# Optimization experiments

Hardware: AMD Instinct MI355X
Metric: run time of the kernel (lower is better)

## Reference

```python
import jax, jax.numpy as jnp
import numpy as np
from jax import lax

R = 4                 # radius (init kwarg)
EPS = 2.0             # eps (init kwarg)
K = 2 * R + 1         # stencil size


def _dir_kernels():
    """8 directional box kernels [8,1,K,K]: L,R,U,D,NW,NE,SW,SE (matches torch construction)."""
    base = np.ones((K, K), np.float32)
    L = base.copy(); L[:, R + 1:] = 0
    Rk = base.copy(); Rk[:, :R] = 0
    U = base.copy(); U[R + 1:, :] = 0
    D = base.copy(); D[:R, :] = 0
    NW = U.copy(); NE = U.copy(); SW = D.copy(); SE = D.copy()
    half = float((R + 1) * (2 * R + 1))
    L, Rk, U, D = L / half, Rk / half, U / half, D / half
    NW[:, R + 1:] = 0; NE[:, :R] = 0; SW[:, R + 1:] = 0; SE[:, :R] = 0
    quad = float((R + 1) ** 2)
    NW, NE, SW, SE = NW / quad, NE / quad, SW / quad, SE / quad
    return jnp.asarray(np.stack([L, Rk, U, D, NW, NE, SW, SE])[:, None])


def _pad(x):
    # ReplicationPad2d(R)
    return jnp.pad(x, ((0, 0), (0, 0), (R, R), (R, R)), mode='edge')


def _conv(x, w, groups=1):
    return lax.conv_general_dilated(
        x, w, window_strides=(1, 1), padding='VALID',
        dimension_numbers=('NCHW', 'OIHW', 'NCHW'), feature_group_count=groups)


def _resize_bilinear_ac(x, H, W):
    """Bilinear resize with align_corners=True, separable gather. x: [N,C,h,w]."""
    n, c, h, w = x.shape
    dt = x.dtype

    def coords(out, src):
        t = jnp.arange(out, dtype=dt) * (jnp.asarray(src - 1, dt) / jnp.asarray(out - 1, dt))
        i0 = jnp.clip(jnp.floor(t).astype(jnp.int32), 0, src - 2)
        f = t - i0.astype(dt)
        return i0, f

    y0, fy = coords(H, h)
    x0, fx = coords(W, w)
    rows = x[:, :, y0, :] * (1 - fy)[None, None, :, None] + x[:, :, y0 + 1, :] * fy[None, None, :, None]
    return rows[:, :, :, x0] * (1 - fx) + rows[:, :, :, x0 + 1] * fx


def setup_inputs() -> dict:
    key = jax.random.key(0)
    k1, k2, k3 = jax.random.split(key, 3)
    lr_x = jax.random.uniform(k1, (1, 3, 256, 256), jnp.float32) * 255.0
    lr_y = jax.random.uniform(k2, (1, 3, 256, 256), jnp.float32) * 255.0
    hr_x = jax.random.uniform(k3, (1, 3, 1024, 1024), jnp.float32) * 255.0
    box_w = jnp.full((3, 1, K, K), 1.0 / (K * K), jnp.float32)  # depthwise box filter weights
    return {"lr_x": lr_x, "lr_y": lr_y, "hr_x": hr_x, "box_w": box_w}


def reference(lr_x, lr_y, hr_x, box_w):
    H, W = hr_x.shape[2], hr_x.shape[3]
    box = lambda t: _conv(_pad(t), box_w, groups=3)

    # --- guided filter coefficients at low res ---
    mean_x = box(lr_x)
    mean_y = box(lr_y)
    cov_xy = box(lr_x * lr_y) - mean_x * mean_y
    var_x = box(lr_x * lr_x) - mean_x * mean_x
    A = cov_xy / (var_x + EPS)
    b = mean_y - A * mean_x

    # --- upsample A, b to hr (bilinear, align_corners=True) ---
    A = _resize_bilinear_ac(A, H, W)
    b = _resize_bilinear_ac(b, H, W)

    # --- 8-direction side-window stencil; channels treated as batch ---
    dirw = _dir_kernels()                      # [8,1,K,K]
    A3 = _pad(A.reshape(3, 1, H, W))
    b3 = _pad(b.reshape(3, 1, H, W))
    im3 = hr_x.reshape(3, 1, H, W)
    cA = _conv(A3, dirw)                       # [3,8,H,W]
    cB = _conv(b3, dirw)                       # [3,8,H,W]
    d = cA * im3 + cB - im3                    # [3,8,H,W]

    idx = jnp.argmin(jnp.abs(d), axis=1, keepdims=True)
    dm = jnp.take_along_axis(d, idx, axis=1)   # min-|delta| direction
    res = (dm + im3).reshape(1, 3, H, W)

    # res.int() truncates toward zero, then clamp(0,255), then float
    return jnp.clip(jnp.trunc(res), 0.0, 255.0)
```

## Files before the change

### kernel.cpp

```cpp
#include <hip/hip_runtime.h>

#define RR 4
#define LRH 256
#define LRW 256
#define HRH 1024
#define HRW 1024

#define LTW 32
#define LTH 8
#define LGW (LTW + 2*RR)
#define LGH (LTH + 2*RR)

#define STW 32
#define STH 32
#define RPT 4
#define SGW (STW + 2*RR)
#define SGH (STH + 2*RR)

__global__ __launch_bounds__(256) void lowres_coeffs(
    const float* __restrict__ lrx, const float* __restrict__ lry,
    float2* __restrict__ AB)
{
    __shared__ float4 sV[LGH][LGW];
    __shared__ float4 sH[LGH][LTW];

    const int c  = blockIdx.z;
    const int X0 = blockIdx.x * LTW, Y0 = blockIdx.y * LTH;
    const int tid = threadIdx.y * LTW + threadIdx.x;
    const float* px = lrx + c * LRH * LRW;
    const float* py = lry + c * LRH * LRW;

    for (int i = tid; i < LGH * LGW; i += 256) {
        int r = i / LGW, col = i - r * LGW;
        int gy = min(max(Y0 - RR + r, 0), LRH - 1);
        int gx = min(max(X0 - RR + col, 0), LRW - 1);
        float xv = px[gy * LRW + gx];
        float yv = py[gy * LRW + gx];
        sV[r][col] = make_float4(xv, yv, xv * yv, xv * xv);
    }
    __syncthreads();

    for (int i = tid; i < LGH * LTW; i += 256) {
        int r = i / LTW, col = i - r * LTW;
        float4 s = sV[r][col];
        #pragma unroll
        for (int k = 1; k < 9; ++k) {
            float4 v = sV[r][col + k];
            s.x += v.x; s.y += v.y; s.z += v.z; s.w += v.w;
        }
        sH[r][col] = s;
    }
    __syncthreads();

    const int tx = threadIdx.x, ty = threadIdx.y;
    float4 s = sH[ty][tx];
    #pragma unroll
    for (int k = 1; k < 9; ++k) {
        float4 v = sH[ty + k][tx];
        s.x += v.x; s.y += v.y; s.z += v.z; s.w += v.w;
    }
    const float inv81 = 1.0f / 81.0f;
    float mx = s.x * inv81, my = s.y * inv81;
    float cov = s.z * inv81 - mx * my;
    float var = s.w * inv81 - mx * mx;
    float A = cov / (var + 2.0f);
    float B = my - A * mx;
    AB[(c * LRH + Y0 + ty) * LRW + X0 + tx] = make_float2(A, B);
}

__global__ __launch_bounds__(256, 4) void stencil_kernel(
    const float2* __restrict__ AB,
    const float* __restrict__ hrx, float* __restrict__ out)
{
    __shared__ float2 sAB[SGH][SGW];
    __shared__ float4 sH[SGH][STW];
    __shared__ int    iLx[SGW];
    __shared__ float2 wLx[SGW];
    __shared__ int    iLyo[SGH];
    __shared__ float2 wLy[SGH];

    const int c  = blockIdx.z;
    const int X0 = blockIdx.x * STW, Y0 = blockIdx.y * STH;
    const int tid = threadIdx.y * STW + threadIdx.x;
    const float2* ABc = AB + c * LRH * LRW;
    const float scale = 255.0f / 1023.0f;

    if (tid < SGW) {
        int gx = min(max(X0 - RR + tid, 0), HRW - 1);
        float t = (float)gx * scale;
        int ix = (int)t; if (ix > LRW - 2) ix = LRW - 2;
        float f = t - (float)ix;
        iLx[tid] = ix;
        wLx[tid] = make_float2(1.0f - f, f);
    } else if (tid >= 64 && tid < 64 + SGH) {
        int r = tid - 64;
        int gy = min(max(Y0 - RR + r, 0), HRH - 1);
        float t = (float)gy * scale;
        int iy = (int)t; if (iy > LRH - 2) iy = LRH - 2;
        float f = t - (float)iy;
        iLyo[r] = iy * LRW;
        wLy[r] = make_float2(1.0f - f, f);
    }
    __syncthreads();

    for (int i = tid; i < SGH * SGW; i += 256) {
        int r = i / SGW, col = i - r * SGW;
        const float2* p = ABc + iLyo[r] + iLx[col];
        float2 wy = wLy[r], wx = wLx[col];
        float2 v00 = p[0], v01 = p[1], v10 = p[LRW], v11 = p[LRW + 1];
        float a0 = v00.x * wy.x + v10.x * wy.y;
        float a1 = v01.x * wy.x + v11.x * wy.y;
        float b0 = v00.y * wy.x + v10.y * wy.y;
        float b1 = v01.y * wy.x + v11.y * wy.y;
        sAB[r][col] = make_float2(a0 * wx.x + a1 * wx.y,
                                  b0 * wx.x + b1 * wx.y);
    }
    __syncthreads();

    for (int i = tid; i < SGH * STW; i += 256) {
        int r = i >> 5, col = i & 31;
        float2 v[9];
        #pragma unroll
        for (int k = 0; k < 9; ++k) v[k] = sAB[r][col + k];
        float hLa = v[0].x + v[1].x + v[2].x + v[3].x + v[4].x;
        float hLb = v[0].y + v[1].y + v[2].y + v[3].y + v[4].y;
        float hRa = v[4].x + v[5].x + v[6].x + v[7].x + v[8].x;
        float hRb = v[4].y + v[5].y + v[6].y + v[7].y + v[8].y;
        sH[r][col] = make_float4(hLa, hLb, hRa, hRb);
    }
    __syncthreads();

    const int tx = threadIdx.x;
    const int base = threadIdx.y * RPT;

    float4 h[RPT + 8];
    float2 cv[RPT + 8];
    #pragma unroll
    for (int k = 0; k < RPT + 8; ++k) {
        h[k]  = sH[base + k][tx];
        cv[k] = sAB[base + k][tx + RR];
    }

    float4 T = h[0], B = h[4];
    float2 Tc = cv[0], Bc = cv[4];
    #pragma unroll
    for (int k = 1; k <= 4; ++k) {
        T.x += h[k].x; T.y += h[k].y; T.z += h[k].z; T.w += h[k].w;
        B.x += h[k+4].x; B.y += h[k+4].y; B.z += h[k+4].z; B.w += h[k+4].w;
        Tc.x += cv[k].x; Tc.y += cv[k].y;
        Bc.x += cv[k+4].x; Bc.y += cv[k+4].y;
    }

    const float i45 = 1.0f / 45.0f, i25 = 1.0f / 25.0f;
    const float* hp = hrx + (c * HRH + Y0 + base) * HRW + X0 + tx;
    float* op = out + (c * HRH + Y0 + base) * HRW + X0 + tx;

    #pragma unroll
    for (int j = 0; j < RPT; ++j) {
        float4 C  = h[j + 4];
        float2 Cc = cv[j + 4];
        float xv = hp[j * HRW];

        float d0 = fmaf(i45, fmaf(T.x + B.x - C.x,  xv, T.y + B.y - C.y),  -xv);
        float d1 = fmaf(i45, fmaf(T.z + B.z - C.z,  xv, T.w + B.w - C.w),  -xv);
        float d2 = fmaf(i45, fmaf(T.x + T.z - Tc.x, xv, T.y + T.w - Tc.y), -xv);
        float d3 = fmaf(i45, fmaf(B.x + B.z - Bc.x, xv, B.y + B.w - Bc.y), -xv);
        float d4 = fmaf(i25, fmaf(T.x, xv, T.y), -xv);
        float d5 = fmaf(i25, fmaf(T.z, xv, T.w), -xv);
        float d6 = fmaf(i25, fmaf(B.x, xv, B.y), -xv);
        float d7 = fmaf(i25, fmaf(B.z, xv, B.w), -xv);

        float a0 = fabsf(d0), a1 = fabsf(d1), a2 = fabsf(d2), a3 = fabsf(d3);
        float a4 = fabsf(d4), a5 = fabsf(d5), a6 = fabsf(d6), a7 = fabsf(d7);
        bool c01 = a0 <= a1; float w01 = c01 ? d0 : d1; float m01 = c01 ? a0 : a1;
        bool c23 = a2 <= a3; float w23 = c23 ? d2 : d3; float m23 = c23 ? a2 : a3;
        bool c45 = a4 <= a5; float w45 = c45 ? d4 : d5; float m45 = c45 ? a4 : a5;
        bool c67 = a6 <= a7; float w67 = c67 ? d6 : d7; float m67 = c67 ? a6 : a7;
        bool cA_ = m01 <= m23; float wA = cA_ ? w01 : w23; float mA = cA_ ? m01 : m23;
        bool cB_ = m45 <= m67; float wB = cB_ ? w45 : w67; float mB = cB_ ? m45 : m67;
        float bd = (mA <= mB) ? wA : wB;

        float res = __builtin_amdgcn_fmed3f(truncf(bd + xv), 0.0f, 255.0f);
        op[j * HRW] = res;

        if (j < RPT - 1) {
            T.x += h[j+5].x - h[j].x;   T.y += h[j+5].y - h[j].y;
            T.z += h[j+5].z - h[j].z;   T.w += h[j+5].w - h[j].w;
            B.x += h[j+9].x - h[j+4].x; B.y += h[j+9].y - h[j+4].y;
            B.z += h[j+9].z - h[j+4].z; B.w += h[j+9].w - h[j+4].w;
            Tc.x += cv[j+5].x - cv[j].x;   Tc.y += cv[j+5].y - cv[j].y;
            Bc.x += cv[j+9].x - cv[j+4].x; Bc.y += cv[j+9].y - cv[j+4].y;
        }
    }
}

extern "C" void kernel_launch(void* const* d_in, const int* in_sizes, int n_in,
                              void* d_out, int out_size, void* d_ws, size_t ws_size,
                              hipStream_t stream) {
    const float* lrx = (const float*)d_in[0];
    const float* lry = (const float*)d_in[1];
    const float* hrx = (const float*)d_in[2];
    (void)d_in[3]; (void)in_sizes; (void)n_in; (void)out_size; (void)ws_size;

    float2* AB = (float2*)d_ws;
    float* outp = (float*)d_out;

    dim3 lblock(LTW, LTH);
    dim3 lgrid(LRW / LTW, LRH / LTH, 3);
    lowres_coeffs<<<lgrid, lblock, 0, stream>>>(lrx, lry, AB);

    dim3 sblock(STW, STH / RPT);
    dim3 sgrid(HRW / STW, HRH / STH, 3);
    stencil_kernel<<<sgrid, sblock, 0, stream>>>(AB, hrx, outp);
}
```

Baseline: 93.54 us.

## Fold bilinear upsampling into directional box sums via precomputed low-res weights

Instead of upsampling A,b to a full high-res halo tile and then box-filtering, the stencil kernel now computes, per output row and column, 4-tap weights that combine the upsample with the half-window box sums. It applies separable vertical weights at low resolution into shared memory (top, bottom and full sums), then horizontal weights per pixel. Tiles grow to 32x64 and occupancy hints rise. This removes the per-tile high-res interpolation and the halo work, but it adds weight-setup loops and different floating-point summation order.

```diff
diff --git a/kernel.cpp b/kernel.cpp
--- a/kernel.cpp
+++ b/kernel.cpp
@@ -1,21 +1,21 @@
 #include <hip/hip_runtime.h>
 
 #define RR 4
-#define LRH 256
-#define LRW 256
-#define HRH 1024
-#define HRW 1024
+#define LRN 256
+#define HRN 1024
+#define SCALE (255.0f/1023.0f)
 
 #define LTW 32
 #define LTH 8
 #define LGW (LTW + 2*RR)
 #define LGH (LTH + 2*RR)
 
-#define STW 32
-#define STH 32
-#define RPT 4
-#define SGW (STW + 2*RR)
-#define SGH (STH + 2*RR)
+#define TX 32
+#define TYR 64
+#define BTH 8
+#define NROW (TYR / BTH)
+#define LRC 12
+#define LRR 20
 
 __global__ __launch_bounds__(256) void lowres_coeffs(
     const float* __restrict__ lrx, const float* __restrict__ lry,
@@ -27,15 +27,15 @@
     const int c  = blockIdx.z;
     const int X0 = blockIdx.x * LTW, Y0 = blockIdx.y * LTH;
     const int tid = threadIdx.y * LTW + threadIdx.x;
-    const float* px = lrx + c * LRH * LRW;
-    const float* py = lry + c * LRH * LRW;
+    const float* px = lrx + c * LRN * LRN;
+    const float* py = lry + c * LRN * LRN;
 
     for (int i = tid; i < LGH * LGW; i += 256) {
         int r = i / LGW, col = i - r * LGW;
-        int gy = min(max(Y0 - RR + r, 0), LRH - 1);
-        int gx = min(max(X0 - RR + col, 0), LRW - 1);
-        float xv = px[gy * LRW + gx];
-        float yv = py[gy * LRW + gx];
+        int gy = min(max(Y0 - RR + r, 0), LRN - 1);
+        int gx = min(max(X0 - RR + col, 0), LRN - 1);
+        float xv = px[gy * LRN + gx];
+        float yv = py[gy * LRN + gx];
         sV[r][col] = make_float4(xv, yv, xv * yv, xv * xv);
     }
     __syncthreads();
@@ -65,110 +65,132 @@
     float var = s.w * inv81 - mx * mx;
     float A = cov / (var + 2.0f);
     float B = my - A * mx;
-    AB[(c * LRH + Y0 + ty) * LRW + X0 + tx] = make_float2(A, B);
-}
-
-__global__ __launch_bounds__(256, 4) void stencil_kernel(
+    AB[(c * LRN + Y0 + ty) * LRN + X0 + tx] = make_float2(A, B);
+}
+
+__device__ inline int anchor_of(int u) {
+    int k = min(max(u - 4, 0), HRN - 1);
+    float t = (float)k * SCALE;
+    int i = (int)t; if (i > LRN - 2) i = LRN - 2;
+    return i;
+}
+
+__device__ inline float4 mkw(int k0, int k1, int a) {
+    float4 w = make_float4(0.f, 0.f, 0.f, 0.f);
+    for (int k = k0; k <= k1; ++k) {
+        int kc = min(max(k, 0), HRN - 1);
+        float t = (float)kc * SCALE;
+        int i = (int)t; if (i > LRN - 2) i = LRN - 2;
+        float f = t - (float)i;
+        int off = i - a;
+        float wa = 1.0f - f, wb = f;
+        w.x += (off == 0) ? wa : 0.0f;
+        w.y += (off == 1) ? wa : ((off == 0) ? wb : 0.0f);
+        w.z += (off == 2) ? wa : ((off == 1) ? wb : 0.0f);
+        w.w += (off == 2) ? wb : 0.0f;
+    }
+    return w;
+}
+
+__global__ __launch_bounds__(256, 6) void stencil_kernel(
     const float2* __restrict__ AB,
     const float* __restrict__ hrx, float* __restrict__ out)
 {
-    __shared__ float2 sAB[SGH][SGW];
-    __shared__ float4 sH[SGH][STW];
-    __shared__ int    iLx[SGW];
-    __shared__ float2 wLx[SGW];
-    __shared__ int    iLyo[SGH];
-    __shared__ float2 wLy[SGH];
+    __shared__ float2 sAB[LRR][LRC];
+    __shared__ float2 sT[TYR][LRC];
+    __shared__ float2 sB[TYR][LRC];
+    __shared__ float2 sF[TYR][LRC];
+    __shared__ float4 sYW[TYR][3];
+    __shared__ int    sYA[TYR];
+    __shared__ float4 sXW[TX][3];
+    __shared__ int    sXA[TX];
 
     const int c  = blockIdx.z;
-    const int X0 = blockIdx.x * STW, Y0 = blockIdx.y * STH;
-    const int tid = threadIdx.y * STW + threadIdx.x;
-    const float2* ABc = AB + c * LRH * LRW;
-    const float scale = 255.0f / 1023.0f;
-
-    if (tid < SGW) {
-        int gx = min(max(X0 - RR + tid, 0), HRW - 1);
-        float t = (float)gx * scale;
-        int ix = (int)t; if (ix > LRW - 2) ix = LRW - 2;
-        float f = t - (float)ix;
-        iLx[tid] = ix;
-        wLx[tid] = make_float2(1.0f - f, f);
-    } else if (tid >= 64 && tid < 64 + SGH) {
+    const int X0 = blockIdx.x * TX, Y0 = blockIdx.y * TYR;
+    const int tid = threadIdx.y * TX + threadIdx.x;
+    const float2* ABc = AB + c * LRN * LRN;
+
+    const int rowbase = anchor_of(Y0);
+    const int colbase = anchor_of(X0);
+
+    if (tid < TX) {
+        int x = X0 + tid;
+        int a = anchor_of(x);
+        sXA[tid] = a - colbase;
+        sXW[tid][0] = mkw(x - 4, x,     a);
+        sXW[tid][1] = mkw(x,     x + 4, a);
+        sXW[tid][2] = mkw(x - 4, x + 4, a);
+    } else if (tid >= 64 && tid < 64 + TYR) {
         int r = tid - 64;
-        int gy = min(max(Y0 - RR + r, 0), HRH - 1);
-        float t = (float)gy * scale;
-        int iy = (int)t; if (iy > LRH - 2) iy = LRH - 2;
-        float f = t - (float)iy;
-        iLyo[r] = iy * LRW;
-        wLy[r] = make_float2(1.0f - f, f);
-    }
-    __syncthreads();
-
-    for (int i = tid; i < SGH * SGW; i += 256) {
-        int r = i / SGW, col = i - r * SGW;
-        const float2* p = ABc + iLyo[r] + iLx[col];
-        float2 wy = wLy[r], wx = wLx[col];
-        float2 v00 = p[0], v01 = p[1], v10 = p[LRW], v11 = p[LRW + 1];
-        float a0 = v00.x * wy.x + v10.x * wy.y;
-        float a1 = v01.x * wy.x + v11.x * wy.y;
-        float b0 = v00.y * wy.x + v10.y * wy.y;
-        float b1 = v01.y * wy.x + v11.y * wy.y;
-        sAB[r][col] = make_float2(a0 * wx.x + a1 * wx.y,
-                                  b0 * wx.x + b1 * wx.y);
-    }
-    __syncthreads();
-
-    for (int i = tid; i < SGH * STW; i += 256) {
-        int r = i >> 5, col = i & 31;
-        float2 v[9];
+        int y = Y0 + r;
+        int a = anchor_of(y);
+        sYA[r] = a - rowbase;
+        sYW[r][0] = mkw(y - 4, y,     a);
+        sYW[r][1] = mkw(y,     y + 4, a);
+        sYW[r][2] = mkw(y - 4, y + 4, a);
+    }
+    for (int i = tid; i < LRR * LRC; i += 256) {
+        int r = i / LRC, cc = i - r * LRC;
+        int gr = min(rowbase + r, LRN - 1);
+        int gc = min(colbase + cc, LRN - 1);
+        sAB[r][cc] = ABc[gr * LRN + gc];
+    }
+    __syncthreads();
+
+    for (int i = tid; i < TYR * LRC; i += 256) {
+        int r = i / LRC, cc = i - r * LRC;
+        int ra = sYA[r];
+        float4 wT = sYW[r][0], wB = sYW[r][1], wF = sYW[r][2];
+        float2 v0 = sAB[ra][cc],     v1 = sAB[ra + 1][cc];
+        float2 v2 = sAB[ra + 2][cc], v3 = sAB[ra + 3][cc];
+        sT[r][cc] = make_float2(wT.x*v0.x + wT.y*v1.x + wT.z*v2.x + wT.w*v3.x,
+                                wT.x*v0.y + wT.y*v1.y + wT.z*v2.y + wT.w*v3.y);
+        sB[r][cc] = make_float2(wB.x*v0.x + wB.y*v1.x + wB.z*v2.x + wB.w*v3.x,
+                                wB.x*v0.y + wB.y*v1.y + wB.z*v2.y + wB.w*v3.y);
+        sF[r][cc] = make_float2(wF.x*v0.x + wF.y*v1.x + wF.z*v2.x + wF.w*v3.x,
+                                wF.x*v0.y + wF.y*v1.y + wF.z*v2.y + wF.w*v3.y);
+    }
+    __syncthreads();
+
+    const int tx = threadIdx.x, tyw = threadIdx.y;
+    const int c0 = sXA[tx];
+    const float4 wL = sXW[tx][0], wR = sXW[tx][1], wFh = sXW[tx][2];
+    const float i45 = 1.0f / 45.0f, i25 = 1.0f / 25.0f;
+    const float* hp = hrx + (c * HRN + Y0 + tyw) * HRN + X0 + tx;
+    float*       op = out + (c * HRN + Y0 + tyw) * HRN + X0 + tx;
+
+    #pragma unroll
+    for (int j = 0; j < NROW; ++j) {
+        const int r = tyw + j * BTH;
+        float LA=0,Lb=0, RA=0,Rb=0, UA=0,Ub=0, DA=0,Db=0;
+        float NWA=0,NWb=0, NEA=0,NEb=0, SWA=0,SWb=0, SEA=0,SEb=0;
         #pragma unroll
-        for (int k = 0; k < 9; ++k) v[k] = sAB[r][col + k];
-        float hLa = v[0].x + v[1].x + v[2].x + v[3].x + v[4].x;
-        float hLb = v[0].y + v[1].y + v[2].y + v[3].y + v[4].y;
-        float hRa = v[4].x + v[5].x + v[6].x + v[7].x + v[8].x;
-        float hRb = v[4].y + v[5].y + v[6].y + v[7].y + v[8].y;
-        sH[r][col] = make_float4(hLa, hLb, hRa, hRb);
-    }
-    __syncthreads();
-
-    const int tx = threadIdx.x;
-    const int base = threadIdx.y * RPT;
-
-    float4 h[RPT + 8];
-    float2 cv[RPT + 8];
-    #pragma unroll
-    for (int k = 0; k < RPT + 8; ++k) {
-        h[k]  = sH[base + k][tx];
-        cv[k] = sAB[base + k][tx + RR];
-    }
-
-    float4 T = h[0], B = h[4];
-    float2 Tc = cv[0], Bc = cv[4];
-    #pragma unroll
-    for (int k = 1; k <= 4; ++k) {
-        T.x += h[k].x; T.y += h[k].y; T.z += h[k].z; T.w += h[k].w;
-        B.x += h[k+4].x; B.y += h[k+4].y; B.z += h[k+4].z; B.w += h[k+4].w;
-        Tc.x += cv[k].x; Tc.y += cv[k].y;
-        Bc.x += cv[k+4].x; Bc.y += cv[k+4].y;
-    }
-
-    const float i45 = 1.0f / 45.0f, i25 = 1.0f / 25.0f;
-    const float* hp = hrx + (c * HRH + Y0 + base) * HRW + X0 + tx;
-    float* op = out + (c * HRH + Y0 + base) * HRW + X0 + tx;
-
-    #pragma unroll
-    for (int j = 0; j < RPT; ++j) {
-        float4 C  = h[j + 4];
-        float2 Cc = cv[j + 4];
-        float xv = hp[j * HRW];
-
-        float d0 = fmaf(i45, fmaf(T.x + B.x - C.x,  xv, T.y + B.y - C.y),  -xv);
-        float d1 = fmaf(i45, fmaf(T.z + B.z - C.z,  xv, T.w + B.w - C.w),  -xv);
-        float d2 = fmaf(i45, fmaf(T.x + T.z - Tc.x, xv, T.y + T.w - Tc.y), -xv);
-        float d3 = fmaf(i45, fmaf(B.x + B.z - Bc.x, xv, B.y + B.w - Bc.y), -xv);
-        float d4 = fmaf(i25, fmaf(T.x, xv, T.y), -xv);
-        float d5 = fmaf(i25, fmaf(T.z, xv, T.w), -xv);
-        float d6 = fmaf(i25, fmaf(B.x, xv, B.y), -xv);
-        float d7 = fmaf(i25, fmaf(B.z, xv, B.w), -xv);
+        for (int k = 0; k < 4; ++k) {
+            float wl = (k==0)?wL.x:(k==1)?wL.y:(k==2)?wL.z:wL.w;
+            float wr = (k==0)?wR.x:(k==1)?wR.y:(k==2)?wR.z:wR.w;
+            float wf = (k==0)?wFh.x:(k==1)?wFh.y:(k==2)?wFh.z:wFh.w;
+            float2 tv = sT[r][c0 + k];
+            float2 bv = sB[r][c0 + k];
+            float2 fv = sF[r][c0 + k];
+            LA = fmaf(wl, fv.x, LA);   Lb = fmaf(wl, fv.y, Lb);
+            RA = fmaf(wr, fv.x, RA);   Rb = fmaf(wr, fv.y, Rb);
+            UA = fmaf(wf, tv.x, UA);   Ub = fmaf(wf, tv.y, Ub);
+            DA = fmaf(wf, bv.x, DA);   Db = fmaf(wf, bv.y, Db);
+            NWA = fmaf(wl, tv.x, NWA); NWb = fmaf(wl, tv.y, NWb);
+            NEA = fmaf(wr, tv.x, NEA); NEb = fmaf(wr, tv.y, NEb);
+            SWA = fmaf(wl, bv.x, SWA); SWb = fmaf(wl, bv.y, SWb);
+            SEA = fmaf(wr, bv.x, SEA); SEb = fmaf(wr, bv.y, SEb);
+        }
+        float xv = hp[j * BTH * HRN];
+
+        float d0 = fmaf(i45, fmaf(LA,  xv, Lb),  -xv);
+        float d1 = fmaf(i45, fmaf(RA,  xv, Rb),  -xv);
+        float d2 = fmaf(i45, fmaf(UA,  xv, Ub),  -xv);
+        float d3 = fmaf(i45, fmaf(DA,  xv, Db),  -xv);
+        float d4 = fmaf(i25, fmaf(NWA, xv, NWb), -xv);
+        float d5 = fmaf(i25, fmaf(NEA, xv, NEb), -xv);
+        float d6 = fmaf(i25, fmaf(SWA, xv, SWb), -xv);
+        float d7 = fmaf(i25, fmaf(SEA, xv, SEb), -xv);
 
         float a0 = fabsf(d0), a1 = fabsf(d1), a2 = fabsf(d2), a3 = fabsf(d3);
         float a4 = fabsf(d4), a5 = fabsf(d5), a6 = fabsf(d6), a7 = fabsf(d7);
@@ -177,20 +199,11 @@
         bool c45 = a4 <= a5; float w45 = c45 ? d4 : d5; float m45 = c45 ? a4 : a5;
         bool c67 = a6 <= a7; float w67 = c67 ? d6 : d7; float m67 = c67 ? a6 : a7;
         bool cA_ = m01 <= m23; float wA = cA_ ? w01 : w23; float mA = cA_ ? m01 : m23;
-        bool cB_ = m45 <= m67; float wB = cB_ ? w45 : w67; float mB = cB_ ? m45 : m67;
-        float bd = (mA <= mB) ? wA : wB;
+        bool cB_ = m45 <= m67; float wB_ = cB_ ? w45 : w67; float mB = cB_ ? m45 : m67;
+        float bd = (mA <= mB) ? wA : wB_;
 
         float res = __builtin_amdgcn_fmed3f(truncf(bd + xv), 0.0f, 255.0f);
-        op[j * HRW] = res;
-
-        if (j < RPT - 1) {
-            T.x += h[j+5].x - h[j].x;   T.y += h[j+5].y - h[j].y;
-            T.z += h[j+5].z - h[j].z;   T.w += h[j+5].w - h[j].w;
-            B.x += h[j+9].x - h[j+4].x; B.y += h[j+9].y - h[j+4].y;
-            B.z += h[j+9].z - h[j+4].z; B.w += h[j+9].w - h[j+4].w;
-            Tc.x += cv[j+5].x - cv[j].x;   Tc.y += cv[j+5].y - cv[j].y;
-            Bc.x += cv[j+9].x - cv[j+4].x; Bc.y += cv[j+9].y - cv[j+4].y;
-        }
+        op[j * BTH * HRN] = res;
     }
 }
 
@@ -206,10 +219,10 @@
     float* outp = (float*)d_out;
 
     dim3 lblock(LTW, LTH);
-    dim3 lgrid(LRW / LTW, LRH / LTH, 3);
+    dim3 lgrid(LRN / LTW, LRN / LTH, 3);
     lowres_coeffs<<<lgrid, lblock, 0, stream>>>(lrx, lry, AB);
 
-    dim3 sblock(STW, STH / RPT);
-    dim3 sgrid(HRW / STW, HRH / STH, 3);
+    dim3 sblock(TX, BTH);
+    dim3 sgrid(HRN / TX, HRN / TYR, 3);
     stencil_kernel<<<sgrid, sblock, 0, stream>>>(AB, hrx, outp);
 }
```

Result: faster. 87.74 us (-6.2%).
